# Optimization experiments

Hardware: AMD Instinct MI355X
Metric: run time of the kernel (lower is better)

## Reference

```python
import itertools
import jax, jax.numpy as jnp
import numpy as np
from jax import lax

B, RES, C = 2048, 7, 512
N = RES * RES            # 49 tokens per window
HEADS = 4
KD = C // 16             # key_dim = 32
D = 4 * KD               # value dim = 128 == C // HEADS
KS = 5                   # dw-conv kernel
EPS = 1e-5


def _bias_idxs():
    pts = list(itertools.product(range(RES), range(RES)))
    offs, idxs = {}, []
    for p1 in pts:
        for p2 in pts:
            o = (abs(p1[0] - p2[0]), abs(p1[1] - p2[1]))
            if o not in offs:
                offs[o] = len(offs)
            idxs.append(offs[o])
    return np.array(idxs, np.int32).reshape(N, N), len(offs)


def setup_inputs() -> dict:
    key = jax.random.key(0)
    k = jax.random.split(key, 20)
    f = jnp.float32
    idxs, noff = _bias_idxs()  # noff == 49 for resolution 7
    qo = 2 * KD + D  # per-head qkv output channels = 192
    return {
        "x": jax.random.normal(k[0], (B, N, C), f),
        "qkv_w": jax.random.normal(k[1], (HEADS, qo, C // HEADS), f) * 0.05,
        "qkv_g": jnp.ones((HEADS, qo), f) + 0.1 * jax.random.normal(k[2], (HEADS, qo), f),
        "qkv_b": 0.1 * jax.random.normal(k[3], (HEADS, qo), f),
        "qkv_m": 0.1 * jax.random.normal(k[4], (HEADS, qo), f),
        "qkv_v": jax.random.uniform(k[5], (HEADS, qo), f, 0.5, 1.5),
        "dw_w": jax.random.normal(k[6], (HEADS, KD, 1, KS, KS), f) * 0.05,
        "dw_g": jnp.ones((HEADS, KD), f) + 0.1 * jax.random.normal(k[7], (HEADS, KD), f),
        "dw_b": 0.1 * jax.random.normal(k[8], (HEADS, KD), f),
        "dw_m": 0.1 * jax.random.normal(k[9], (HEADS, KD), f),
        "dw_v": jax.random.uniform(k[10], (HEADS, KD), f, 0.5, 1.5),
        "proj_w": jax.random.normal(k[11], (C, HEADS * D), f) * 0.05,
        "proj_g": jnp.ones((C,), f) + 0.1 * jax.random.normal(k[12], (C,), f),
        "proj_b": 0.1 * jax.random.normal(k[13], (C,), f),
        "proj_m": 0.1 * jax.random.normal(k[14], (C,), f),
        "proj_v": jax.random.uniform(k[15], (C,), f, 0.5, 1.5),
        "attn_bias": 0.1 * jax.random.normal(k[16], (HEADS, noff), f),
        "bias_idxs": jnp.asarray(idxs),
    }


def _bn(y, g, b, m, v):
    # inference-mode BatchNorm folded as per-channel affine (channels last)
    return (y - m) * (g * jax.lax.rsqrt(v + EPS)) + b


def reference(x, qkv_w, qkv_g, qkv_b, qkv_m, qkv_v,
              dw_w, dw_g, dw_b, dw_m, dw_v,
              proj_w, proj_g, proj_b, proj_m, proj_v,
              attn_bias, bias_idxs):
    scale = KD ** -0.5
    ab = attn_bias[:, bias_idxs]               # [HEADS, N, N] relative-position bias
    chunks = jnp.split(x, HEADS, axis=-1)      # per-head input chunks [B, N, C/HEADS]
    feat = chunks[0]
    outs = []
    for i in range(HEADS):
        if i > 0:
            feat = feat + chunks[i]            # cascade: prev head output + next chunk
        y = jnp.einsum('bnc,oc->bno', feat, qkv_w[i])
        y = _bn(y, qkv_g[i], qkv_b[i], qkv_m[i], qkv_v[i])   # [B, N, 192]
        q, k, v = y[..., :KD], y[..., KD:2 * KD], y[..., 2 * KD:]
        # depthwise 5x5 conv on q over the 7x7 window
        qi = q.reshape(B, RES, RES, KD)
        w = jnp.transpose(dw_w[i], (2, 3, 1, 0))  # OIHW(groups) -> HWIO [5,5,1,KD]
        qi = lax.conv_general_dilated(qi, w, (1, 1), 'SAME',
                                      feature_group_count=KD,
                                      dimension_numbers=('NHWC', 'HWIO', 'NHWC'))
        qi = _bn(qi, dw_g[i], dw_b[i], dw_m[i], dw_v[i])
        q = qi.reshape(B, N, KD)
        attn = jnp.einsum('bnk,bmk->bnm', q, k) * scale + ab[i]  # [B, N, N]
        attn = jax.nn.softmax(attn, axis=-1)
        feat = jnp.einsum('bnm,bmd->bnd', attn, v)               # [B, N, D]
        outs.append(feat)
    h = jax.nn.relu(jnp.concatenate(outs, axis=-1))              # [B, N, HEADS*D]
    out = jnp.einsum('bnd,od->bno', h, proj_w)
    out = _bn(out, proj_g, proj_b, proj_m, proj_v)               # [B, N, C]
    return out
```

## Files before the change

### kernel.cpp

```cpp
#include <hip/hip_runtime.h>
#include <hip/hip_bf16.h>

#define BATCH 2048
#define RES   7
#define NPOS  49
#define CDIM  512
#define HEADS 4
#define KD    32
#define DDIM  128
#define QO    192
#define EPS   1e-5f

#define FS 132
#define QS 36
#define AS 68
#define VS 68

typedef __attribute__((ext_vector_type(8))) short short8;
typedef __attribute__((ext_vector_type(4))) float floatx4;

union S8u { short8 v; __hip_bfloat162 h[4]; };

__device__ inline short8 pack_bf16x8(float4 a, float4 b) {
    S8u u;
    u.h[0] = __float22bfloat162_rn(make_float2(a.x, a.y));
    u.h[1] = __float22bfloat162_rn(make_float2(a.z, a.w));
    u.h[2] = __float22bfloat162_rn(make_float2(b.x, b.y));
    u.h[3] = __float22bfloat162_rn(make_float2(b.z, b.w));
    return u.v;
}

__device__ inline void split_pack8(float4 a, float4 b, short8& hi, short8& lo) {
    S8u H, L;
    float v0[8] = {a.x, a.y, a.z, a.w, b.x, b.y, b.z, b.w};
    #pragma unroll
    for (int p = 0; p < 4; ++p) {
        __hip_bfloat162 hp = __float22bfloat162_rn(make_float2(v0[2*p], v0[2*p+1]));
        float h0 = __bfloat162float(hp.x);
        float h1 = __bfloat162float(hp.y);
        H.h[p] = hp;
        L.h[p] = __float22bfloat162_rn(make_float2(v0[2*p] - h0, v0[2*p+1] - h1));
    }
    hi = H.v; lo = L.v;
}

#define MFMA(a, b, c) __builtin_amdgcn_mfma_f32_16x16x32_bf16((a), (b), (c), 0, 0, 0)

__global__ __launch_bounds__(512, 2) void fused_cga_kernel(
    const float* __restrict__ x,
    const float* __restrict__ qkv_w,
    const float* __restrict__ qkv_g,  const float* __restrict__ qkv_bb,
    const float* __restrict__ qkv_m,  const float* __restrict__ qkv_v,
    const float* __restrict__ dw_w,
    const float* __restrict__ dw_g,   const float* __restrict__ dw_bb,
    const float* __restrict__ dw_m,   const float* __restrict__ dw_v,
    const float* __restrict__ proj_w,
    const float* __restrict__ proj_g, const float* __restrict__ proj_bb,
    const float* __restrict__ proj_m, const float* __restrict__ proj_v,
    const float* __restrict__ attn_bias,
    const int*   __restrict__ bias_idxs,
    float* __restrict__ out)
{
    __shared__ float feat[64 * FS];
    __shared__ float qbuf[64 * QS];
    __shared__ float qcv [64 * QS];
    __shared__ float kbuf[64 * QS];
    __shared__ float Wu  [6144];
    __shared__ float U2  [128 * VS];
    __shared__ float sq[QO], tq[QO];
    __shared__ float wdw[KD * 25], sdw[KD], tdw[KD];

    float* att = Wu;
    unsigned short* qkvh = (unsigned short*)Wu;
    unsigned short* qkvl = qkvh + QO * 32;
    float* vT = U2;
    unsigned short* Bl = (unsigned short*)U2;

    const int b    = blockIdx.x;
    const int tid  = threadIdx.x;
    const int lane = tid & 63;
    const int wid  = tid >> 6;
    const int quad = lane >> 4;
    const int l15  = lane & 15;
    const int mt   = wid & 3;
    const int nh   = wid >> 2;

    const float* xb = x + (size_t)b * NPOS * CDIM;

    floatx4 po[16];
    #pragma unroll
    for (int t = 0; t < 16; ++t) po[t] = (floatx4){0.f, 0.f, 0.f, 0.f};

    for (int i = tid; i < 15 * FS; i += 512) feat[49 * FS + i] = 0.f;

    for (int head = 0; head < HEADS; ++head) {
        for (int i = tid; i < NPOS * (DDIM / 4); i += 512) {
            int n = i >> 5, c4 = i & 31;
            float4 xv = *(const float4*)(xb + n * CDIM + head * DDIM + c4 * 4);
            float* fp = feat + n * FS + c4 * 4;
            if (head == 0) { *(float4*)fp = xv; }
            else {
                float4 f = *(float4*)fp;
                f.x += xv.x; f.y += xv.y; f.z += xv.z; f.w += xv.w;
                *(float4*)fp = f;
            }
        }
        if (tid < QO) {
            float s = qkv_g[head * QO + tid] * rsqrtf(qkv_v[head * QO + tid] + EPS);
            sq[tid] = s;
            tq[tid] = qkv_bb[head * QO + tid] - qkv_m[head * QO + tid] * s;
        } else if (tid < QO + KD) {
            int ch = tid - QO;
            float s = dw_g[head * KD + ch] * rsqrtf(dw_v[head * KD + ch] + EPS);
            sdw[ch] = s;
            tdw[ch] = dw_bb[head * KD + ch] - dw_m[head * KD + ch] * s;
        }
        for (int i = tid; i < KD * 25; i += 512) wdw[i] = dw_w[head * KD * 25 + i];
        __syncthreads();

        {
            floatx4 qa[6];
            #pragma unroll
            for (int t = 0; t < 6; ++t) qa[t] = (floatx4){0.f, 0.f, 0.f, 0.f};
            for (int ks = 0; ks < 4; ++ks) {
                for (int i = tid; i < QO * 4; i += 512) {
                    int rowi = i >> 2, j8 = i & 3;
                    const float* wp = qkv_w + (size_t)(head * QO + rowi) * DDIM + ks * 32 + j8 * 8;
                    short8 h8, l8;
                    split_pack8(*(const float4*)wp, *(const float4*)(wp + 4), h8, l8);
                    *(short8*)(qkvh + rowi * 32 + j8 * 8) = h8;
                    *(short8*)(qkvl + rowi * 32 + j8 * 8) = l8;
                }
                __syncthreads();
                const float* ap = feat + (mt * 16 + l15) * FS + ks * 32 + quad * 8;
                short8 ah, al;
                split_pack8(*(const float4*)ap, *(const float4*)(ap + 4), ah, al);
                #pragma unroll
                for (int t = 0; t < 6; ++t) {
                    int rw = (nh * 96 + t * 16 + l15) * 32 + quad * 8;
                    short8 bh = *(const short8*)(qkvh + rw);
                    short8 bl = *(const short8*)(qkvl + rw);
                    qa[t] = MFMA(ah, bh, qa[t]);
                    qa[t] = MFMA(al, bh, qa[t]);
                    qa[t] = MFMA(ah, bl, qa[t]);
                }
                __syncthreads();
            }
            #pragma unroll
            for (int t = 0; t < 6; ++t) {
                int o = nh * 96 + t * 16 + l15;
                float s = sq[o], tt = tq[o];
                #pragma unroll
                for (int r = 0; r < 4; ++r) {
                    int row = mt * 16 + quad * 4 + r;
                    if (row < NPOS) {
                        float y = qa[t][r] * s + tt;
                        if (o < KD)          qbuf[row * QS + o] = y;
                        else if (o < 2 * KD) kbuf[row * QS + (o - KD)] = y;
                        else                 vT[(o - 2 * KD) * VS + row] = y;
                    }
                }
            }
        }
        __syncthreads();

        for (int i = tid; i < NPOS * KD; i += 512) {
            int n = i >> 5, ch = i & 31;
            int rr = n / RES, cc = n - rr * RES;
            float acc = 0.f;
            #pragma unroll
            for (int dy = 0; dy < 5; ++dy) {
                int ry = rr + dy - 2;
                if (ry < 0 || ry >= RES) continue;
                #pragma unroll
                for (int dx = 0; dx < 5; ++dx) {
                    int cx = cc + dx - 2;
                    if (cx < 0 || cx >= RES) continue;
                    acc += qbuf[(ry * RES + cx) * QS + ch] * wdw[ch * 25 + dy * 5 + dx];
                }
            }
            qcv[n * QS + ch] = acc * sdw[ch] + tdw[ch];
        }
        __syncthreads();

        {
            floatx4 sa[2];
            sa[0] = (floatx4){0.f, 0.f, 0.f, 0.f};
            sa[1] = (floatx4){0.f, 0.f, 0.f, 0.f};
            const float* ap = qcv + (mt * 16 + l15) * QS + quad * 8;
            short8 ah, al;
            split_pack8(*(const float4*)ap, *(const float4*)(ap + 4), ah, al);
            #pragma unroll
            for (int t = 0; t < 2; ++t) {
                const float* kp = kbuf + ((nh * 2 + t) * 16 + l15) * QS + quad * 8;
                short8 bh, bl;
                split_pack8(*(const float4*)kp, *(const float4*)(kp + 4), bh, bl);
                sa[t] = MFMA(ah, bh, sa[t]);
                sa[t] = MFMA(al, bh, sa[t]);
                sa[t] = MFMA(ah, bl, sa[t]);
            }
            const float scale = 0.17677669529663687f;
            #pragma unroll
            for (int t = 0; t < 2; ++t) {
                int nn = (nh * 2 + t) * 16 + l15;
                #pragma unroll
                for (int r = 0; r < 4; ++r) {
                    int row = mt * 16 + quad * 4 + r;
                    if (row < NPOS) {
                        if (nn < NPOS)
                            att[row * AS + nn] = sa[t][r] * scale
                                + attn_bias[head * NPOS + bias_idxs[row * NPOS + nn]];
                        else if (nn < 64)
                            att[row * AS + nn] = 0.f;
                    }
                }
            }
        }
        __syncthreads();

        {
            int row = tid >> 3, g = tid & 7;
            if (row < NPOS) {
                float mx = -1e30f;
                for (int n = g; n < NPOS; n += 8) mx = fmaxf(mx, att[row * AS + n]);
                #pragma unroll
                for (int d = 1; d < 8; d <<= 1) mx = fmaxf(mx, __shfl_xor(mx, d));
                float sm = 0.f;
                for (int n = g; n < NPOS; n += 8) {
                    float e = __expf(att[row * AS + n] - mx);
                    att[row * AS + n] = e;
                    sm += e;
                }
                #pragma unroll
                for (int d = 1; d < 8; d <<= 1) sm += __shfl_xor(sm, d);
                float inv = 1.f / sm;
                for (int n = g; n < NPOS; n += 8) att[row * AS + n] *= inv;
            }
            for (int i = tid; i < 128 * 19; i += 512) {
                int d = i / 19, m2 = i - d * 19 + 49;
                vT[d * VS + m2] = 0.f;
            }
        }
        __syncthreads();

        {
            floatx4 pa[4];
            #pragma unroll
            for (int t = 0; t < 4; ++t) pa[t] = (floatx4){0.f, 0.f, 0.f, 0.f};
            #pragma unroll
            for (int ks = 0; ks < 2; ++ks) {
                const float* ap = att + (mt * 16 + l15) * AS + ks * 32 + quad * 8;
                short8 ah, al;
                split_pack8(*(const float4*)ap, *(const float4*)(ap + 4), ah, al);
                #pragma unroll
                for (int t = 0; t < 4; ++t) {
                    const float* vp = vT + ((nh * 4 + t) * 16 + l15) * VS + ks * 32 + quad * 8;
                    short8 bh, bl;
                    split_pack8(*(const float4*)vp, *(const float4*)(vp + 4), bh, bl);
                    pa[t] = MFMA(ah, bh, pa[t]);
                    pa[t] = MFMA(al, bh, pa[t]);
                    pa[t] = MFMA(ah, bl, pa[t]);
                }
            }
            #pragma unroll
            for (int t = 0; t < 4; ++t) {
                int d = (nh * 4 + t) * 16 + l15;
                #pragma unroll
                for (int r = 0; r < 4; ++r) {
                    int row = mt * 16 + quad * 4 + r;
                    if (row < NPOS) feat[row * FS + d] = pa[t][r];
                }
            }
        }
        __syncthreads();

        for (int ks = 0; ks < 4; ++ks) {
            for (int it = tid; it < CDIM * 8; it += 512) {
                int rowi = it >> 3, j4 = it & 7;
                float4 w = *(const float4*)(proj_w + (size_t)rowi * CDIM + head * DDIM + ks * 32 + j4 * 4);
                __hip_bfloat162 p0 = __float22bfloat162_rn(make_float2(w.x, w.y));
                __hip_bfloat162 p1 = __float22bfloat162_rn(make_float2(w.z, w.w));
                unsigned short* dp = Bl + rowi * 32 + j4 * 4;
                *(__hip_bfloat162*)dp       = p0;
                *(__hip_bfloat162*)(dp + 2) = p1;
            }
            __syncthreads();
            {
                const float* ap = feat + (mt * 16 + l15) * FS + ks * 32 + quad * 8;
                float4 a0 = *(const float4*)ap;
                float4 a1 = *(const float4*)(ap + 4);
                a0.x = fmaxf(a0.x, 0.f); a0.y = fmaxf(a0.y, 0.f);
                a0.z = fmaxf(a0.z, 0.f); a0.w = fmaxf(a0.w, 0.f);
                a1.x = fmaxf(a1.x, 0.f); a1.y = fmaxf(a1.y, 0.f);
                a1.z = fmaxf(a1.z, 0.f); a1.w = fmaxf(a1.w, 0.f);
                short8 af = pack_bf16x8(a0, a1);
                #pragma unroll
                for (int t = 0; t < 16; ++t) {
                    short8 bf = *(const short8*)(Bl + ((nh * 256 + t * 16 + l15) << 5) + quad * 8);
                    po[t] = __builtin_amdgcn_mfma_f32_16x16x32_bf16(af, bf, po[t], 0, 0, 0);
                }
            }
            __syncthreads();
        }
    }

    float* sp = U2;
    float* tp = U2 + 512;
    {
        int o = tid;
        float s = proj_g[o] * rsqrtf(proj_v[o] + EPS);
        sp[o] = s;
        tp[o] = proj_bb[o] - proj_m[o] * s;
    }
    __syncthreads();
    #pragma unroll
    for (int t = 0; t < 16; ++t) {
        int o = nh * 256 + t * 16 + l15;
        float s = sp[o], tt = tp[o];
        #pragma unroll
        for (int r = 0; r < 4; ++r) {
            int row = mt * 16 + quad * 4 + r;
            if (row < NPOS)
                out[((size_t)b * NPOS + row) * CDIM + o] = po[t][r] * s + tt;
        }
    }
}

extern "C" void kernel_launch(void* const* d_in, const int* in_sizes, int n_in,
                              void* d_out, int out_size, void* d_ws, size_t ws_size,
                              hipStream_t stream) {
    const float* x      = (const float*)d_in[0];
    const float* qkv_w  = (const float*)d_in[1];
    const float* qkv_g  = (const float*)d_in[2];
    const float* qkv_b  = (const float*)d_in[3];
    const float* qkv_m  = (const float*)d_in[4];
    const float* qkv_v  = (const float*)d_in[5];
    const float* dw_w   = (const float*)d_in[6];
    const float* dw_g   = (const float*)d_in[7];
    const float* dw_b   = (const float*)d_in[8];
    const float* dw_m   = (const float*)d_in[9];
    const float* dw_v   = (const float*)d_in[10];
    const float* proj_w = (const float*)d_in[11];
    const float* proj_g = (const float*)d_in[12];
    const float* proj_b = (const float*)d_in[13];
    const float* proj_m = (const float*)d_in[14];
    const float* proj_v = (const float*)d_in[15];
    const float* attn_bias = (const float*)d_in[16];
    const int*   bias_idxs = (const int*)d_in[17];
    float* out = (float*)d_out;
    (void)d_ws; (void)ws_size;

    hipLaunchKernelGGL(fused_cga_kernel, dim3(BATCH), dim3(512), 0, stream,
        x, qkv_w, qkv_g, qkv_b, qkv_m, qkv_v,
        dw_w, dw_g, dw_b, dw_m, dw_v,
        proj_w, proj_g, proj_b, proj_m, proj_v,
        attn_bias, bias_idxs, out);
}
```

Measured before the change: 1.148 ms.

## Stream weights directly from global into MFMA fragments and shrink shared memory

Drops the per-k-step staging of qkv and proj weights through LDS, along with its barriers. Each wave now loads and converts its B fragments straight from global memory (L2-cached), and proj is retiled so each wave owns 64 output columns across all row tiles. V is pre-split into bf16 hi/lo once when the qkv output is stored, instead of being re-split on every PV fragment load. Shared buffers are overlaid into one smaller arena and launch bounds are raised to 4 blocks per CU for occupancy. The cost is more redundant global weight traffic, recomputing the BN constants per thread, and more register pressure under the tighter launch bound.

```diff
diff --git a/kernel.cpp b/kernel.cpp
--- a/kernel.cpp
+++ b/kernel.cpp
@@ -11,15 +11,24 @@
 #define QO    192
 #define EPS   1e-5f
 
-#define FS 132
-#define QS 36
-#define AS 68
-#define VS 68
+#define FSTR 132
+#define QSTR 36
+#define ASTR 68
+#define VSTR 72
+
+#define OFF_QCV  0
+#define OFF_ATT  7056
+#define OFF_QBUF 25872
+#define OFF_KBUF 32928
+#define OFF_VTH  39984
+#define OFF_VTL  58416
+#define SMEM_SZ  76848
 
 typedef __attribute__((ext_vector_type(8))) short short8;
 typedef __attribute__((ext_vector_type(4))) float floatx4;
 
 union S8u { short8 v; __hip_bfloat162 h[4]; };
+union BU  { __hip_bfloat16 b; unsigned short u; };
 
 __device__ inline short8 pack_bf16x8(float4 a, float4 b) {
     S8u u;
@@ -46,7 +55,7 @@
 
 #define MFMA(a, b, c) __builtin_amdgcn_mfma_f32_16x16x32_bf16((a), (b), (c), 0, 0, 0)
 
-__global__ __launch_bounds__(512, 2) void fused_cga_kernel(
+__global__ __launch_bounds__(512, 4) void fused_cga_kernel(
     const float* __restrict__ x,
     const float* __restrict__ qkv_w,
     const float* __restrict__ qkv_g,  const float* __restrict__ qkv_bb,
@@ -61,20 +70,14 @@
     const int*   __restrict__ bias_idxs,
     float* __restrict__ out)
 {
-    __shared__ float feat[64 * FS];
-    __shared__ float qbuf[64 * QS];
-    __shared__ float qcv [64 * QS];
-    __shared__ float kbuf[64 * QS];
-    __shared__ float Wu  [6144];
-    __shared__ float U2  [128 * VS];
-    __shared__ float sq[QO], tq[QO];
-    __shared__ float wdw[KD * 25], sdw[KD], tdw[KD];
-
-    float* att = Wu;
-    unsigned short* qkvh = (unsigned short*)Wu;
-    unsigned short* qkvl = qkvh + QO * 32;
-    float* vT = U2;
-    unsigned short* Bl = (unsigned short*)U2;
+    __shared__ __align__(16) unsigned char smem[SMEM_SZ];
+    float* feat = (float*)smem;
+    float* qcv  = (float*)(smem + OFF_QCV);
+    float* att  = (float*)(smem + OFF_ATT);
+    float* qbuf = (float*)(smem + OFF_QBUF);
+    float* kbuf = (float*)(smem + OFF_KBUF);
+    unsigned short* vTh = (unsigned short*)(smem + OFF_VTH);
+    unsigned short* vTl = (unsigned short*)(smem + OFF_VTL);
 
     const int b    = blockIdx.x;
     const int tid  = threadIdx.x;
@@ -91,13 +94,17 @@
     #pragma unroll
     for (int t = 0; t < 16; ++t) po[t] = (floatx4){0.f, 0.f, 0.f, 0.f};
 
-    for (int i = tid; i < 15 * FS; i += 512) feat[49 * FS + i] = 0.f;
+    for (int i = tid; i < 128 * 15; i += 512) {
+        int d = i / 15, c = 49 + (i - d * 15);
+        vTh[d * VSTR + c] = 0;
+        vTl[d * VSTR + c] = 0;
+    }
 
     for (int head = 0; head < HEADS; ++head) {
         for (int i = tid; i < NPOS * (DDIM / 4); i += 512) {
             int n = i >> 5, c4 = i & 31;
             float4 xv = *(const float4*)(xb + n * CDIM + head * DDIM + c4 * 4);
-            float* fp = feat + n * FS + c4 * 4;
+            float* fp = feat + n * FSTR + c4 * 4;
             if (head == 0) { *(float4*)fp = xv; }
             else {
                 float4 f = *(float4*)fp;
@@ -105,17 +112,6 @@
                 *(float4*)fp = f;
             }
         }
-        if (tid < QO) {
-            float s = qkv_g[head * QO + tid] * rsqrtf(qkv_v[head * QO + tid] + EPS);
-            sq[tid] = s;
-            tq[tid] = qkv_bb[head * QO + tid] - qkv_m[head * QO + tid] * s;
-        } else if (tid < QO + KD) {
-            int ch = tid - QO;
-            float s = dw_g[head * KD + ch] * rsqrtf(dw_v[head * KD + ch] + EPS);
-            sdw[ch] = s;
-            tdw[ch] = dw_bb[head * KD + ch] - dw_m[head * KD + ch] * s;
-        }
-        for (int i = tid; i < KD * 25; i += 512) wdw[i] = dw_w[head * KD * 25 + i];
         __syncthreads();
 
         {
@@ -123,41 +119,44 @@
             #pragma unroll
             for (int t = 0; t < 6; ++t) qa[t] = (floatx4){0.f, 0.f, 0.f, 0.f};
             for (int ks = 0; ks < 4; ++ks) {
-                for (int i = tid; i < QO * 4; i += 512) {
-                    int rowi = i >> 2, j8 = i & 3;
-                    const float* wp = qkv_w + (size_t)(head * QO + rowi) * DDIM + ks * 32 + j8 * 8;
-                    short8 h8, l8;
-                    split_pack8(*(const float4*)wp, *(const float4*)(wp + 4), h8, l8);
-                    *(short8*)(qkvh + rowi * 32 + j8 * 8) = h8;
-                    *(short8*)(qkvl + rowi * 32 + j8 * 8) = l8;
-                }
-                __syncthreads();
-                const float* ap = feat + (mt * 16 + l15) * FS + ks * 32 + quad * 8;
+                const float* ap = feat + (mt * 16 + l15) * FSTR + ks * 32 + quad * 8;
                 short8 ah, al;
                 split_pack8(*(const float4*)ap, *(const float4*)(ap + 4), ah, al);
                 #pragma unroll
                 for (int t = 0; t < 6; ++t) {
-                    int rw = (nh * 96 + t * 16 + l15) * 32 + quad * 8;
-                    short8 bh = *(const short8*)(qkvh + rw);
-                    short8 bl = *(const short8*)(qkvl + rw);
+                    const float* wp = qkv_w
+                        + (size_t)(head * QO + nh * 96 + t * 16 + l15) * DDIM + ks * 32 + quad * 8;
+                    short8 bh, bl;
+                    split_pack8(*(const float4*)wp, *(const float4*)(wp + 4), bh, bl);
                     qa[t] = MFMA(ah, bh, qa[t]);
                     qa[t] = MFMA(al, bh, qa[t]);
                     qa[t] = MFMA(ah, bl, qa[t]);
                 }
-                __syncthreads();
             }
             #pragma unroll
             for (int t = 0; t < 6; ++t) {
-                int o = nh * 96 + t * 16 + l15;
-                float s = sq[o], tt = tq[o];
+                int o   = nh * 96 + t * 16 + l15;
+                int idx = head * QO + o;
+                float s  = qkv_g[idx] * rsqrtf(qkv_v[idx] + EPS);
+                float tt = qkv_bb[idx] - qkv_m[idx] * s;
                 #pragma unroll
                 for (int r = 0; r < 4; ++r) {
                     int row = mt * 16 + quad * 4 + r;
                     if (row < NPOS) {
                         float y = qa[t][r] * s + tt;
-                        if (o < KD)          qbuf[row * QS + o] = y;
-                        else if (o < 2 * KD) kbuf[row * QS + (o - KD)] = y;
-                        else                 vT[(o - 2 * KD) * VS + row] = y;
+                        if (o < KD)          qbuf[row * QSTR + o] = y;
+                        else if (o < 2 * KD) kbuf[row * QSTR + (o - KD)] = y;
+                        else {
+                            int d = o - 2 * KD;
+                            BU hu, lu;
+                            __hip_bfloat162 hp = __float22bfloat162_rn(make_float2(y, 0.f));
+                            hu.b = hp.x;
+                            float hf = __bfloat162float(hp.x);
+                            __hip_bfloat162 lp = __float22bfloat162_rn(make_float2(y - hf, 0.f));
+                            lu.b = lp.x;
+                            vTh[d * VSTR + row] = hu.u;
+                            vTl[d * VSTR + row] = lu.u;
+                        }
                     }
                 }
             }
@@ -167,6 +166,7 @@
         for (int i = tid; i < NPOS * KD; i += 512) {
             int n = i >> 5, ch = i & 31;
             int rr = n / RES, cc = n - rr * RES;
+            const float* wd = dw_w + (size_t)(head * KD + ch) * 25;
             float acc = 0.f;
             #pragma unroll
             for (int dy = 0; dy < 5; ++dy) {
@@ -176,10 +176,13 @@
                 for (int dx = 0; dx < 5; ++dx) {
                     int cx = cc + dx - 2;
                     if (cx < 0 || cx >= RES) continue;
-                    acc += qbuf[(ry * RES + cx) * QS + ch] * wdw[ch * 25 + dy * 5 + dx];
-                }
-            }
-            qcv[n * QS + ch] = acc * sdw[ch] + tdw[ch];
+                    acc += qbuf[(ry * RES + cx) * QSTR + ch] * wd[dy * 5 + dx];
+                }
+            }
+            int idx = head * KD + ch;
+            float s  = dw_g[idx] * rsqrtf(dw_v[idx] + EPS);
+            float tt = dw_bb[idx] - dw_m[idx] * s;
+            qcv[n * QSTR + ch] = acc * s + tt;
         }
         __syncthreads();
 
@@ -187,12 +190,12 @@
             floatx4 sa[2];
             sa[0] = (floatx4){0.f, 0.f, 0.f, 0.f};
             sa[1] = (floatx4){0.f, 0.f, 0.f, 0.f};
-            const float* ap = qcv + (mt * 16 + l15) * QS + quad * 8;
+            const float* ap = qcv + (mt * 16 + l15) * QSTR + quad * 8;
             short8 ah, al;
             split_pack8(*(const float4*)ap, *(const float4*)(ap + 4), ah, al);
             #pragma unroll
             for (int t = 0; t < 2; ++t) {
-                const float* kp = kbuf + ((nh * 2 + t) * 16 + l15) * QS + quad * 8;
+                const float* kp = kbuf + ((nh * 2 + t) * 16 + l15) * QSTR + quad * 8;
                 short8 bh, bl;
                 split_pack8(*(const float4*)kp, *(const float4*)(kp + 4), bh, bl);
                 sa[t] = MFMA(ah, bh, sa[t]);
@@ -208,10 +211,10 @@
                     int row = mt * 16 + quad * 4 + r;
                     if (row < NPOS) {
                         if (nn < NPOS)
-                            att[row * AS + nn] = sa[t][r] * scale
+                            att[row * ASTR + nn] = sa[t][r] * scale
                                 + attn_bias[head * NPOS + bias_idxs[row * NPOS + nn]];
-                        else if (nn < 64)
-                            att[row * AS + nn] = 0.f;
+                        else
+                            att[row * ASTR + nn] = 0.f;
                     }
                 }
             }
@@ -222,44 +225,44 @@
             int row = tid >> 3, g = tid & 7;
             if (row < NPOS) {
                 float mx = -1e30f;
-                for (int n = g; n < NPOS; n += 8) mx = fmaxf(mx, att[row * AS + n]);
+                for (int n = g; n < NPOS; n += 8) mx = fmaxf(mx, att[row * ASTR + n]);
                 #pragma unroll
                 for (int d = 1; d < 8; d <<= 1) mx = fmaxf(mx, __shfl_xor(mx, d));
                 float sm = 0.f;
                 for (int n = g; n < NPOS; n += 8) {
-                    float e = __expf(att[row * AS + n] - mx);
-                    att[row * AS + n] = e;
+                    float e = __expf(att[row * ASTR + n] - mx);
+                    att[row * ASTR + n] = e;
                     sm += e;
                 }
                 #pragma unroll
                 for (int d = 1; d < 8; d <<= 1) sm += __shfl_xor(sm, d);
                 float inv = 1.f / sm;
-                for (int n = g; n < NPOS; n += 8) att[row * AS + n] *= inv;
-            }
-            for (int i = tid; i < 128 * 19; i += 512) {
-                int d = i / 19, m2 = i - d * 19 + 49;
-                vT[d * VS + m2] = 0.f;
-            }
-        }
-        __syncthreads();
-
-        {
+                for (int n = g; n < NPOS; n += 8) att[row * ASTR + n] *= inv;
+            }
+        }
+        __syncthreads();
+
+        {
+            short8 ah[2], al[2];
+            #pragma unroll
+            for (int ks = 0; ks < 2; ++ks) {
+                const float* ap = att + (mt * 16 + l15) * ASTR + ks * 32 + quad * 8;
+                split_pack8(*(const float4*)ap, *(const float4*)(ap + 4), ah[ks], al[ks]);
+            }
+            __syncthreads();
             floatx4 pa[4];
             #pragma unroll
             for (int t = 0; t < 4; ++t) pa[t] = (floatx4){0.f, 0.f, 0.f, 0.f};
             #pragma unroll
             for (int ks = 0; ks < 2; ++ks) {
-                const float* ap = att + (mt * 16 + l15) * AS + ks * 32 + quad * 8;
-                short8 ah, al;
-                split_pack8(*(const float4*)ap, *(const float4*)(ap + 4), ah, al);
                 #pragma unroll
                 for (int t = 0; t < 4; ++t) {
-                    const float* vp = vT + ((nh * 4 + t) * 16 + l15) * VS + ks * 32 + quad * 8;
-                    short8 bh, bl;
-                    split_pack8(*(const float4*)vp, *(const float4*)(vp + 4), bh, bl);
-                    pa[t] = MFMA(ah, bh, pa[t]);
-                    pa[t] = MFMA(al, bh, pa[t]);
-                    pa[t] = MFMA(ah, bl, pa[t]);
+                    int off = ((nh * 4 + t) * 16 + l15) * VSTR + ks * 32 + quad * 8;
+                    short8 bh = *(const short8*)(vTh + off);
+                    short8 bl = *(const short8*)(vTl + off);
+                    pa[t] = MFMA(ah[ks], bh, pa[t]);
+                    pa[t] = MFMA(al[ks], bh, pa[t]);
+                    pa[t] = MFMA(ah[ks], bl, pa[t]);
                 }
             }
             #pragma unroll
@@ -268,60 +271,57 @@
                 #pragma unroll
                 for (int r = 0; r < 4; ++r) {
                     int row = mt * 16 + quad * 4 + r;
-                    if (row < NPOS) feat[row * FS + d] = pa[t][r];
-                }
-            }
-        }
-        __syncthreads();
-
-        for (int ks = 0; ks < 4; ++ks) {
-            for (int it = tid; it < CDIM * 8; it += 512) {
-                int rowi = it >> 3, j4 = it & 7;
-                float4 w = *(const float4*)(proj_w + (size_t)rowi * CDIM + head * DDIM + ks * 32 + j4 * 4);
-                __hip_bfloat162 p0 = __float22bfloat162_rn(make_float2(w.x, w.y));
-                __hip_bfloat162 p1 = __float22bfloat162_rn(make_float2(w.z, w.w));
-                unsigned short* dp = Bl + rowi * 32 + j4 * 4;
-                *(__hip_bfloat162*)dp       = p0;
-                *(__hip_bfloat162*)(dp + 2) = p1;
-            }
-            __syncthreads();
-            {
-                const float* ap = feat + (mt * 16 + l15) * FS + ks * 32 + quad * 8;
-                float4 a0 = *(const float4*)ap;
-                float4 a1 = *(const float4*)(ap + 4);
-                a0.x = fmaxf(a0.x, 0.f); a0.y = fmaxf(a0.y, 0.f);
-                a0.z = fmaxf(a0.z, 0.f); a0.w = fmaxf(a0.w, 0.f);
-                a1.x = fmaxf(a1.x, 0.f); a1.y = fmaxf(a1.y, 0.f);
-                a1.z = fmaxf(a1.z, 0.f); a1.w = fmaxf(a1.w, 0.f);
-                short8 af = pack_bf16x8(a0, a1);
-                #pragma unroll
-                for (int t = 0; t < 16; ++t) {
-                    short8 bf = *(const short8*)(Bl + ((nh * 256 + t * 16 + l15) << 5) + quad * 8);
-                    po[t] = __builtin_amdgcn_mfma_f32_16x16x32_bf16(af, bf, po[t], 0, 0, 0);
-                }
-            }
-            __syncthreads();
-        }
+                    if (row < NPOS) feat[row * FSTR + d] = pa[t][r];
+                }
+            }
+        }
+        __syncthreads();
+
+        {
+            const int nbase = wid * 64;
+            for (int ks = 0; ks < 4; ++ks) {
+                short8 af[4];
+                #pragma unroll
+                for (int mm = 0; mm < 4; ++mm) {
+                    const float* ap = feat + (mm * 16 + l15) * FSTR + ks * 32 + quad * 8;
+                    float4 a0 = *(const float4*)ap;
+                    float4 a1 = *(const float4*)(ap + 4);
+                    a0.x = fmaxf(a0.x, 0.f); a0.y = fmaxf(a0.y, 0.f);
+                    a0.z = fmaxf(a0.z, 0.f); a0.w = fmaxf(a0.w, 0.f);
+                    a1.x = fmaxf(a1.x, 0.f); a1.y = fmaxf(a1.y, 0.f);
+                    a1.z = fmaxf(a1.z, 0.f); a1.w = fmaxf(a1.w, 0.f);
+                    af[mm] = pack_bf16x8(a0, a1);
+                }
+                #pragma unroll
+                for (int j = 0; j < 4; ++j) {
+                    const float* wp = proj_w
+                        + (size_t)(nbase + j * 16 + l15) * CDIM + head * DDIM + ks * 32 + quad * 8;
+                    short8 bf = pack_bf16x8(*(const float4*)wp, *(const float4*)(wp + 4));
+                    #pragma unroll
+                    for (int mm = 0; mm < 4; ++mm)
+                        po[mm * 4 + j] = MFMA(af[mm], bf, po[mm * 4 + j]);
+                }
+            }
+        }
+        __syncthreads();
     }
 
-    float* sp = U2;
-    float* tp = U2 + 512;
     {
-        int o = tid;
-        float s = proj_g[o] * rsqrtf(proj_v[o] + EPS);
-        sp[o] = s;
-        tp[o] = proj_bb[o] - proj_m[o] * s;
-    }
-    __syncthreads();
-    #pragma unroll
-    for (int t = 0; t < 16; ++t) {
-        int o = nh * 256 + t * 16 + l15;
-        float s = sp[o], tt = tp[o];
+        const int nbase = wid * 64;
         #pragma unroll
-        for (int r = 0; r < 4; ++r) {
-            int row = mt * 16 + quad * 4 + r;
-            if (row < NPOS)
-                out[((size_t)b * NPOS + row) * CDIM + o] = po[t][r] * s + tt;
+        for (int j = 0; j < 4; ++j) {
+            int o = nbase + j * 16 + l15;
+            float s  = proj_g[o] * rsqrtf(proj_v[o] + EPS);
+            float tt = proj_bb[o] - proj_m[o] * s;
+            #pragma unroll
+            for (int mm = 0; mm < 4; ++mm) {
+                #pragma unroll
+                for (int r = 0; r < 4; ++r) {
+                    int row = mm * 16 + quad * 4 + r;
+                    if (row < NPOS)
+                        out[((size_t)b * NPOS + row) * CDIM + o] = po[mm * 4 + j][r] * s + tt;
+                }
+            }
         }
     }
 }
```

Result: slower. 1.481 ms (+29.0%).
